# Optimization experiments

Hardware: AMD Instinct MI355X
Metric: run time of the kernel (lower is better)

Reference implementation:

```python
import jax, jax.numpy as jnp
import numpy as np

B, NUM_CLASSES, H, W, CF = 2, 19, 64, 64, 256
TOPK_IDX = 20  # hard-coded in the torch source: sorted descending value at index 20


def _cosine(x):
    # x: [B, N, D] -> clamped cosine affinity [B, N, N]
    xn = x / (jnp.linalg.norm(x, axis=2, keepdims=True) + 1e-9)
    return jnp.maximum(jnp.einsum('bnd,bmd->bnm', xn, xn), 0.0)


def _conv1x1(x, w, b):
    # x: [B, C, H, W], w: [O, C], b: [O]
    return jnp.einsum('bchw,oc->bohw', x, w) + b[None, :, None, None]


def setup_inputs() -> dict:
    key = jax.random.key(0)
    ks = jax.random.split(key, 12)
    s_c = (2.0 / NUM_CLASSES) ** 0.5  # kaiming fan_in scale for 1x1 conv
    s_f = (2.0 / CF) ** 0.5
    return {
        'pred': jax.random.normal(ks[0], (B, NUM_CLASSES, H, W), jnp.float32),
        'feat': jax.random.normal(ks[1], (B, CF, H, W), jnp.float32),
        'w_cls1': jax.random.normal(ks[2], (NUM_CLASSES, NUM_CLASSES), jnp.float32) * s_c,
        'b_cls1': jnp.zeros((NUM_CLASSES,), jnp.float32),
        'w_cls2': jax.random.normal(ks[3], (NUM_CLASSES, NUM_CLASSES), jnp.float32) * s_c,
        'b_cls2': jnp.zeros((NUM_CLASSES,), jnp.float32),
        'w_pro1': jax.random.normal(ks[4], (CF, CF), jnp.float32) * s_f,
        'b_pro1': jnp.zeros((CF,), jnp.float32),
        'w_pro2': jax.random.normal(ks[5], (CF, CF), jnp.float32) * s_f,
        'b_pro2': jnp.zeros((CF,), jnp.float32),
        'class_weight': jnp.ones((NUM_CLASSES,), jnp.float32),
    }


def reference(pred, feat, w_cls1, b_cls1, w_cls2, b_cls2,
              w_pro1, b_pro1, w_pro2, b_pro2, class_weight):
    bsz, c, h, w = feat.shape
    C = pred.shape[1]
    N = h * w
    feat_flat = feat.reshape(bsz, c, N).transpose(0, 2, 1)  # [B, N, 256]

    # --- no_grad block 1: confidence mask + top-k sparsified cosine affinity ---
    prob = jax.nn.softmax(pred, axis=1)
    p_prob = prob.max(axis=1)      # [B, H, W]
    p_max = prob.argmax(axis=1)    # [B, H, W]
    cwm = class_weight / (class_weight.max() + 1e-10) * 0.95
    mask = ((p_prob >= 0.95) | (p_prob >= cwm[p_max])).astype(jnp.float32)
    mask = jax.lax.stop_gradient(mask.reshape(bsz, N, 1))  # broadcast over classes

    aff1 = _cosine(feat_flat)                                # [B, N, N]
    thr = -jnp.sort(-aff1, axis=-1)[:, :, TOPK_IDX:TOPK_IDX + 1]  # per-row 21st largest
    aff1 = jnp.where(aff1 < thr, 0.0, aff1)
    aff1 = jax.lax.stop_gradient(aff1 + aff1.transpose(0, 2, 1))

    # --- degree-normalized propagation of predictions ---
    pred_flat = pred.reshape(bsz, C, N).transpose(0, 2, 1)   # [B, N, C]
    d1 = (aff1.sum(-1) + 1e-10) ** -0.5                      # D^{-1/2}
    aff1n = d1[:, :, None] * aff1 * d1[:, None, :]           # D^{-1/2} A D^{-1/2}
    p2 = jnp.einsum('bnm,bmc->bnc', aff1n, pred_flat)
    p3 = (0.8 * p2 + 0.2 * pred_flat) * (1.0 - mask) + (0.2 * p2 + 0.8 * pred_flat) * mask
    pred2 = p3.transpose(0, 2, 1).reshape(bsz, C, h, w)
    pred_out = _conv1x1(_conv1x1(pred2, w_cls1, b_cls1), w_cls2, b_cls2)

    # --- no_grad block 2: class-consistency-masked affinity over refined softmax ---
    oh = jax.nn.one_hot(p_max, C, dtype=jnp.float32)         # [B, H, W, C]
    # faithful to torch: permute(0,2,3,1) on the already-[B,H,W,C] one-hot, then flat view
    oh = jnp.transpose(oh, (0, 2, 3, 1)).reshape(bsz, -1, C)
    sp = jax.nn.softmax(pred_out, axis=1).reshape(bsz, C, N).transpose(0, 2, 1)
    aff_f = _cosine(sp)
    aff_f = jnp.where(_cosine(oh) == 0.0, 0.0, aff_f)
    d2 = (aff_f.sum(-1) + 1e-10) ** -0.5
    aff_fn = jax.lax.stop_gradient(d2[:, :, None] * aff_f * d2[:, None, :])

    # --- propagate features and project ---
    new_feat = jnp.einsum('bnm,bmc->bnc', aff_fn, feat_flat)
    new_feat = new_feat.transpose(0, 2, 1).reshape(bsz, c, h, w)
    feat_out = _conv1x1(jax.nn.relu(_conv1x1(new_feat, w_pro1, b_pro1)), w_pro2, b_pro2)
    return pred_out, feat_out
```

## Files before the change

kernel.cpp:

```cpp
#include <hip/hip_runtime.h>

#define NN 4096
#define DD 256
#define CC 19
#define BB 2
#define KSPLIT 4

typedef __attribute__((ext_vector_type(8))) short bf16x8;
typedef _Float16 f16x8 __attribute__((ext_vector_type(8)));
typedef __attribute__((ext_vector_type(4))) float f32x4;

#define GLL16(gp, lp) __builtin_amdgcn_global_load_lds( \
    (const __attribute__((address_space(1))) unsigned int*)(gp), \
    (__attribute__((address_space(3))) unsigned int*)(lp), 16, 0, 0)

__device__ inline unsigned short f2b(float f) {
  unsigned int u = __float_as_uint(f);
  return (unsigned short)((u + 0x7FFFu + ((u >> 16) & 1u)) >> 16);
}
__device__ inline float b2f(unsigned short h) {
  return __uint_as_float(((unsigned int)h) << 16);
}
__device__ inline unsigned int pack2(float a, float b) {
  return (unsigned int)f2b(a) | ((unsigned int)f2b(b) << 16);
}
__device__ inline void split16(float x, unsigned short& h, unsigned short& l) {
  _Float16 hh = (_Float16)x;
  float hf = (float)hh;
  _Float16 ll = (_Float16)((x - hf) * 2048.0f);
  h = *reinterpret_cast<unsigned short*>(&hh);
  l = *reinterpret_cast<unsigned short*>(&ll);
}

__global__ void k_mask_bits(const float* __restrict__ pred, const float* __restrict__ cw,
                            float* __restrict__ maskb, unsigned int* __restrict__ ohbits) {
  int g = blockIdx.x * 256 + threadIdx.x;
  if (g >= BB * NN) return;
  int b = g >> 12, n = g & (NN - 1);
  const float* p = pred + (size_t)b * CC * NN + n;
  float v[CC];
  float mx = -1e30f; int am = 0;
#pragma unroll
  for (int c = 0; c < CC; ++c) {
    float t = p[(size_t)c * NN];
    v[c] = t;
    if (t > mx) { mx = t; am = c; }
  }
  float s = 0.f;
#pragma unroll
  for (int c = 0; c < CC; ++c) s += expf(v[c] - mx);
  float pprob = 1.f / s;
  float cmax = 0.f;
#pragma unroll
  for (int c = 0; c < CC; ++c) cmax = fmaxf(cmax, cw[c]);
  float cwm = cw[am] / (cmax + 1e-10f) * 0.95f;
  maskb[g] = (pprob >= 0.95f || pprob >= cwm) ? 1.f : 0.f;
  int h = n >> 6, w = n & 63;
  int L = w * (CC * 64) + am * 64 + h;
  atomicOr(&ohbits[b * NN + L / CC], 1u << (L % CC));
}

__global__ void k_norm_feat(const float* __restrict__ feat,
                            unsigned short* __restrict__ xh, unsigned short* __restrict__ xl) {
  int g = blockIdx.x * 64 + threadIdx.x;
  int b = g >> 12, n = g & (NN - 1);
  const float* f = feat + (size_t)b * DD * NN + n;
  float s = 0.f;
  for (int d = 0; d < DD; ++d) { float t = f[(size_t)d * NN]; s += t * t; }
  float r = 1.f / (sqrtf(s) + 1e-9f);
  size_t ob = ((size_t)b * NN + n) * DD;
  for (int d = 0; d < DD; d += 4) {
    ushort4 oh, ol;
    split16(f[(size_t)d * NN] * r, oh.x, ol.x);
    split16(f[(size_t)(d + 1) * NN] * r, oh.y, ol.y);
    split16(f[(size_t)(d + 2) * NN] * r, oh.z, ol.z);
    split16(f[(size_t)(d + 3) * NN] * r, oh.w, ol.w);
    *reinterpret_cast<ushort4*>(&xh[ob + d]) = oh;
    *reinterpret_cast<ushort4*>(&xl[ob + d]) = ol;
  }
}

__global__ __launch_bounds__(256, 2) void k_gram1(const unsigned short* __restrict__ xh,
                                                  const unsigned short* __restrict__ xl,
                                                  float* __restrict__ M) {
  int L = blockIdx.x;
  int b = blockIdx.y;
  int I = 0;
  while (L >= 32 - I) { L -= 32 - I; ++I; }
  int J = I + L;
  int i0 = I * 128, j0 = J * 128;
  float* Mb = M + (size_t)b * NN * NN;
  const unsigned short* XH = xh + (size_t)b * NN * DD;
  const unsigned short* XL = xl + (size_t)b * NN * DD;
  __shared__ unsigned short stage[2][4][128][32];
  int t = threadIdx.x;
  int wave = t >> 6, lane = t & 63;
  int wr = (wave & 1) * 64, wc = (wave >> 1) * 64;
  int lrow = lane & 15, quad = lane >> 4;
  int sel = (lrow >> 1) & 3;
  f32x4 accH[4][4] = {}, accL[4][4] = {};
  const unsigned short* src = (wave == 0) ? XH + (size_t)i0 * DD
                             : (wave == 1) ? XL + (size_t)i0 * DD
                             : (wave == 2) ? XH + (size_t)j0 * DD
                                           : XL + (size_t)j0 * DD;
  int srow = lane >> 2;
  int spart = (lane & 3) ^ ((lane >> 3) & 3);
#pragma unroll
  for (int e = 0; e < 8; ++e)
    GLL16(&src[(size_t)(e * 16 + srow) * DD + spart * 8], &stage[0][wave][e * 16][0]);
  __syncthreads();
  int cur = 0;
  for (int k0 = 0; k0 < DD; k0 += 32) {
    if (k0 + 32 < DD) {
#pragma unroll
      for (int e = 0; e < 8; ++e)
        GLL16(&src[(size_t)(e * 16 + srow) * DD + k0 + 32 + spart * 8],
              &stage[cur ^ 1][wave][e * 16][0]);
    }
    f16x8 ah[4], al[4], bh[4], bl[4];
#pragma unroll
    for (int i = 0; i < 4; ++i) {
      int ra = wr + i * 16 + lrow;
      int rb = wc + i * 16 + lrow;
      int sl = (quad ^ sel) * 8;
      ah[i] = *reinterpret_cast<const f16x8*>(&stage[cur][0][ra][sl]);
      al[i] = *reinterpret_cast<const f16x8*>(&stage[cur][1][ra][sl]);
      bh[i] = *reinterpret_cast<const f16x8*>(&stage[cur][2][rb][sl]);
      bl[i] = *reinterpret_cast<const f16x8*>(&stage[cur][3][rb][sl]);
    }
#pragma unroll
    for (int i = 0; i < 4; ++i) {
#pragma unroll
      for (int j = 0; j < 4; ++j) {
        accH[i][j] = __builtin_amdgcn_mfma_f32_16x16x32_f16(ah[i], bh[j], accH[i][j], 0, 0, 0);
        accL[i][j] = __builtin_amdgcn_mfma_f32_16x16x32_f16(ah[i], bl[j], accL[i][j], 0, 0, 0);
        accL[i][j] = __builtin_amdgcn_mfma_f32_16x16x32_f16(al[i], bh[j], accL[i][j], 0, 0, 0);
      }
    }
    __syncthreads();
    cur ^= 1;
  }
#pragma unroll
  for (int i = 0; i < 4; ++i)
#pragma unroll
    for (int j = 0; j < 4; ++j)
#pragma unroll
      for (int reg = 0; reg < 4; ++reg)
        accH[i][j][reg] = fmaxf(accH[i][j][reg] + accL[i][j][reg] * 4.8828125e-4f, 0.f);
  float* buf = (float*)stage;
  int rr = t >> 4, cc = t & 15;
  for (int half = 0; half < 2; ++half) {
    __syncthreads();
    if ((wr >> 6) == half) {
#pragma unroll
      for (int i = 0; i < 4; ++i)
#pragma unroll
        for (int j = 0; j < 4; ++j)
#pragma unroll
          for (int reg = 0; reg < 4; ++reg)
            buf[(i * 16 + quad * 4 + reg) * 132 + wc + j * 16 + lrow] = accH[i][j][reg];
    }
    __syncthreads();
#pragma unroll
    for (int i = 0; i < 4; ++i) {
      int row = rr + i * 16;
#pragma unroll
      for (int q = 0; q < 2; ++q) {
        int col = cc * 4 + q * 64;
        *reinterpret_cast<float4*>(&Mb[(size_t)(i0 + half * 64 + row) * NN + j0 + col]) =
            *reinterpret_cast<float4*>(&buf[row * 132 + col]);
      }
    }
  }
  if (I != J) {
    for (int half = 0; half < 2; ++half) {
      __syncthreads();
      if ((wc >> 6) == half) {
#pragma unroll
        for (int i = 0; i < 4; ++i)
#pragma unroll
          for (int j = 0; j < 4; ++j)
#pragma unroll
            for (int reg = 0; reg < 4; ++reg)
              buf[(j * 16 + lrow) * 132 + wr + i * 16 + quad * 4 + reg] = accH[i][j][reg];
      }
      __syncthreads();
#pragma unroll
      for (int i = 0; i < 4; ++i) {
        int row = rr + i * 16;
#pragma unroll
        for (int q = 0; q < 2; ++q) {
          int col = cc * 4 + q * 64;
          *reinterpret_cast<float4*>(&Mb[(size_t)(j0 + half * 64 + row) * NN + i0 + col]) =
              *reinterpret_cast<float4*>(&buf[row * 132 + col]);
        }
      }
    }
  }
}

__global__ __launch_bounds__(256, 2) void k_topk(const float* __restrict__ M,
                                                 float* __restrict__ thr) {
  __shared__ unsigned int cbuf[4][64];
  int b = blockIdx.y;
  int wave = threadIdx.x >> 6, lane = threadIdx.x & 63;
  int n = blockIdx.x * 4 + wave;
  const float* row = M + (size_t)b * NN * NN + (size_t)n * NN;
  uint4 v[16];
#pragma unroll
  for (int e = 0; e < 16; ++e) {
    unsigned long long addr = (unsigned long long)(row + lane * 4 + e * 256);
    asm volatile("global_load_dwordx4 %0, %1, off" : "=v"(v[e]) : "v"(addr));
  }
  asm volatile("s_waitcnt vmcnt(0)" ::: "memory");
  __builtin_amdgcn_sched_barrier(0);
  unsigned int mx = 0u;
#pragma unroll
  for (int e = 0; e < 16; ++e) {
    unsigned int a = v[e].x > v[e].y ? v[e].x : v[e].y;
    unsigned int c2 = v[e].z > v[e].w ? v[e].z : v[e].w;
    a = a > c2 ? a : c2;
    mx = mx > a ? mx : a;
  }
  unsigned int lo = 0u, hi = 0x3FC00000u;
  while (lo < hi) {
    unsigned int mid = lo + ((hi - lo + 1) >> 1);
    if (__popcll(__ballot(mx >= mid)) >= 21) lo = mid; else hi = mid - 1;
  }
  unsigned int s = lo;
  unsigned int base = 0;
  unsigned long long ltmask = (1ull << lane) - 1ull;
#pragma unroll
  for (int e = 0; e < 16; ++e) {
#pragma unroll
    for (int q = 0; q < 4; ++q) {
      unsigned int val = (q == 0) ? v[e].x : (q == 1) ? v[e].y : (q == 2) ? v[e].z : v[e].w;
      unsigned long long mk = __ballot(val >= s);
      if (mk) {
        unsigned int pos = base + (unsigned int)__popcll(mk & ltmask);
        if (val >= s && pos < 64u) cbuf[wave][pos] = val;
        base += (unsigned int)__popcll(mk);
      }
    }
  }
  asm volatile("s_waitcnt lgkmcnt(0)" ::: "memory");
  __builtin_amdgcn_sched_barrier(0);
  unsigned int t = s;
  if (base <= 64u) {
    unsigned int cand = (lane < (int)base) ? cbuf[wave][lane] : 0u;
    lo = s; hi = 0x3FC00000u;
    while (lo < hi) {
      unsigned int mid = lo + ((hi - lo + 1) >> 1);
      if (__popcll(__ballot(cand >= mid)) >= 21) lo = mid; else hi = mid - 1;
    }
    t = lo;
  }
  {
    unsigned int t1 = t + 1u;
    int c1 = 0, c2 = 0;
#pragma unroll
    for (int e = 0; e < 16; ++e) {
      c1 += (int)__popcll(__ballot(v[e].x >= t));
      c1 += (int)__popcll(__ballot(v[e].y >= t));
      c1 += (int)__popcll(__ballot(v[e].z >= t));
      c1 += (int)__popcll(__ballot(v[e].w >= t));
      c2 += (int)__popcll(__ballot(v[e].x >= t1));
      c2 += (int)__popcll(__ballot(v[e].y >= t1));
      c2 += (int)__popcll(__ballot(v[e].z >= t1));
      c2 += (int)__popcll(__ballot(v[e].w >= t1));
    }
    if (!(c1 >= 21 && c2 < 21)) {
      lo = 0u; hi = 0x40000000u;
      while (lo < hi) {
        unsigned int mid = lo + ((hi - lo + 1) >> 1);
        int c = 0;
#pragma unroll
        for (int e = 0; e < 16; ++e) {
          c += (int)__popcll(__ballot(v[e].x >= mid));
          c += (int)__popcll(__ballot(v[e].y >= mid));
          c += (int)__popcll(__ballot(v[e].z >= mid));
          c += (int)__popcll(__ballot(v[e].w >= mid));
        }
        if (c >= 21) lo = mid; else hi = mid - 1;
      }
      t = lo;
    }
  }
  if (lane == 0) thr[b * NN + n] = __uint_as_float(t);
}

__global__ __launch_bounds__(256) void k_symm(float* __restrict__ M, const float* __restrict__ thr,
                                              float* __restrict__ dsum) {
  int L = blockIdx.x;
  int b = blockIdx.y;
  int I = 0;
  while (L >= 64 - I) { L -= 64 - I; ++I; }
  int J = I + L;
  float* Mb = M + (size_t)b * NN * NN;
  unsigned short* Mus = (unsigned short*)Mb;
  const float* th = thr + b * NN;
  __shared__ float A[64][65];
  int t = threadIdx.x;
  int i0 = I * 64, j0 = J * 64;
  float areg[16];
#pragma unroll
  for (int e = 0; e < 16; ++e) {
    int lin = t + e * 256;
    int i = lin >> 6, j = lin & 63;
    areg[e] = Mb[(size_t)(i0 + i) * NN + j0 + j];
  }
#pragma unroll
  for (int e = 0; e < 16; ++e) {
    int lin = t + e * 256;
    int i = lin >> 6, j = lin & 63;
    float a = areg[e];
    float v = a * ((a >= th[i0 + i] ? 1.f : 0.f) + (a >= th[j0 + j] ? 1.f : 0.f));
    A[i][j] = v;
  }
  __syncthreads();
  {
    int i = t >> 2, seg = (t & 3) * 16;
    float v[16];
#pragma unroll
    for (int q = 0; q < 4; ++q)
      *reinterpret_cast<float4*>(&v[q * 4]) = *reinterpret_cast<float4*>(&A[i][seg + q * 4]);
    unsigned int pk[8];
#pragma unroll
    for (int q = 0; q < 8; ++q) pk[q] = pack2(v[2 * q], v[2 * q + 1]);
    size_t ub = 2 * (size_t)(i0 + i) * NN + 2 * (size_t)j0 + seg;
    *reinterpret_cast<int4*>(&Mus[ub])     = *reinterpret_cast<int4*>(&pk[0]);
    *reinterpret_cast<int4*>(&Mus[ub + 8]) = *reinterpret_cast<int4*>(&pk[4]);
  }
  if (I != J) {
    int j = t >> 2, seg = (t & 3) * 16;
    float v[16];
#pragma unroll
    for (int e = 0; e < 16; ++e) v[e] = A[seg + e][j];
    unsigned int pk[8];
#pragma unroll
    for (int q = 0; q < 8; ++q) pk[q] = pack2(v[2 * q], v[2 * q + 1]);
    size_t ub = 2 * (size_t)(j0 + j) * NN + 2 * (size_t)i0 + seg;
    *reinterpret_cast<int4*>(&Mus[ub])     = *reinterpret_cast<int4*>(&pk[0]);
    *reinterpret_cast<int4*>(&Mus[ub + 8]) = *reinterpret_cast<int4*>(&pk[4]);
  }
  if (t < 64) {
    float s = 0.f;
#pragma unroll
    for (int j = 0; j < 64; ++j) s += A[t][j];
    atomicAdd(&dsum[b * NN + i0 + t], s);
  } else if (t < 128 && I != J) {
    int j = t - 64;
    float s = 0.f;
#pragma unroll
    for (int i = 0; i < 64; ++i) s += A[i][j];
    atomicAdd(&dsum[b * NN + j0 + j], s);
  }
}

__global__ void k_fin_d(float* __restrict__ d) {
  int g = blockIdx.x * 256 + threadIdx.x;
  if (g < BB * NN) d[g] = 1.f / sqrtf(d[g] + 1e-10f);
}

__global__ void k_make_yb(const float* __restrict__ pred, const float* __restrict__ d1,
                          unsigned short* __restrict__ ybh) {
  int g = blockIdx.x * 256 + threadIdx.x;
  int idx = g * 4;
  int b = idx / (32 * NN);
  int c = (idx / NN) & 31;
  int n = idx & (NN - 1);
  ushort4 o = make_ushort4(0, 0, 0, 0);
  if (c < CC) {
    float4 p = *reinterpret_cast<const float4*>(&pred[((size_t)b * CC + c) * NN + n]);
    const float* dd = d1 + b * NN + n;
    o.x = f2b(p.x * dd[0]); o.y = f2b(p.y * dd[1]);
    o.z = f2b(p.z * dd[2]); o.w = f2b(p.w * dd[3]);
  }
  *reinterpret_cast<ushort4*>(&ybh[idx]) = o;
}

__global__ __launch_bounds__(256) void k_p2_mfma(
    const float* __restrict__ M, const unsigned short* __restrict__ ybh,
    const float* __restrict__ d1, float* __restrict__ p2b) {
  int b = blockIdx.y;
  int n0 = blockIdx.x * 64;
  const unsigned short* Mus = (const unsigned short*)(M + (size_t)b * NN * NN);
  const unsigned short* Y = ybh + (size_t)b * 32 * NN;
  __shared__ unsigned short As[64][72];
  __shared__ unsigned short Ys[32][72];
  int t = threadIdx.x;
  int wave = t >> 6, lane = t & 63;
  int wn = (wave & 1) * 32;
  int wc = (wave >> 1) * 16;
  int lrow = lane & 15, quad = lane >> 4;
  f32x4 acc[2] = {{0.f,0.f,0.f,0.f},{0.f,0.f,0.f,0.f}};
  int sr = t >> 3, scc = (t & 7) * 8;
  for (int m0 = 0; m0 < NN; m0 += 64) {
#pragma unroll
    for (int e = 0; e < 2; ++e) {
      int rr = sr + e * 32;
      *reinterpret_cast<int4*>(&As[rr][scc]) =
          *reinterpret_cast<const int4*>(&Mus[2 * (size_t)(n0 + rr) * NN + 2 * (size_t)m0 + scc]);
    }
    *reinterpret_cast<int4*>(&Ys[sr][scc]) =
        *reinterpret_cast<const int4*>(&Y[(size_t)sr * NN + m0 + scc]);
    __syncthreads();
#pragma unroll
    for (int kc = 0; kc < 2; ++kc) {
      int ko = kc * 32 + quad * 8;
      bf16x8 bfr = *reinterpret_cast<const bf16x8*>(&Ys[wc + lrow][ko]);
#pragma unroll
      for (int i = 0; i < 2; ++i) {
        bf16x8 af = *reinterpret_cast<const bf16x8*>(&As[wn + i * 16 + lrow][ko]);
        acc[i] = __builtin_amdgcn_mfma_f32_16x16x32_bf16(af, bfr, acc[i], 0, 0, 0);
      }
    }
    __syncthreads();
  }
  int c = wc + lrow;
  if (c < CC) {
#pragma unroll
    for (int i = 0; i < 2; ++i) {
#pragma unroll
      for (int reg = 0; reg < 4; ++reg) {
        int n = n0 + wn + i * 16 + quad * 4 + reg;
        p2b[((size_t)b * NN + n) * CC + c] = d1[b * NN + n] * acc[i][reg];
      }
    }
  }
}

__global__ __launch_bounds__(256) void k_pred_head(const float* __restrict__ pred,
    const float* __restrict__ p2b, const float* __restrict__ maskb,
    const float* __restrict__ w1, const float* __restrict__ b1,
    const float* __restrict__ w2, const float* __restrict__ b2,
    float* __restrict__ out, float* __restrict__ spnT) {
  __shared__ float sw1[CC * CC], sw2[CC * CC], sb1[CC], sb2[CC];
  int t = threadIdx.x;
  for (int i = t; i < CC * CC; i += 256) { sw1[i] = w1[i]; sw2[i] = w2[i]; }
  if (t < CC) { sb1[t] = b1[t]; sb2[t] = b2[t]; }
  __syncthreads();
  int g = blockIdx.x * 256 + t;
  int b = g >> 12, n = g & (NN - 1);
  float m = maskb[g];
  float ca = (m > 0.5f) ? 0.2f : 0.8f;
  float cb = (m > 0.5f) ? 0.8f : 0.2f;
  const float* P = pred + (size_t)b * CC * NN + n;
  const float* Q = p2b + (size_t)g * CC;
  float p3[CC];
#pragma unroll
  for (int c = 0; c < CC; ++c) p3[c] = ca * Q[c] + cb * P[(size_t)c * NN];
  float midv[CC];
#pragma unroll
  for (int o = 0; o < CC; ++o) {
    float s = sb1[o];
#pragma unroll
    for (int c = 0; c < CC; ++c) s += sw1[o * CC + c] * p3[c];
    midv[o] = s;
  }
  float ov[CC];
  float mx = -1e30f;
#pragma unroll
  for (int o = 0; o < CC; ++o) {
    float s = sb2[o];
#pragma unroll
    for (int c = 0; c < CC; ++c) s += sw2[o * CC + c] * midv[c];
    ov[o] = s;
    out[(size_t)b * CC * NN + (size_t)o * NN + n] = s;
    mx = fmaxf(mx, s);
  }
  float se = 0.f;
  float e[CC];
#pragma unroll
  for (int o = 0; o < CC; ++o) { e[o] = expf(ov[o] - mx); se += e[o]; }
  float inv = 1.f / se;
  float nrm = 0.f;
#pragma unroll
  for (int o = 0; o < CC; ++o) { float sp = e[o] * inv; e[o] = sp; nrm += sp * sp; }
  float rn = 1.f / (sqrtf(nrm) + 1e-9f);
#pragma unroll
  for (int o = 0; o < CC; ++o) spnT[(size_t)b * CC * NN + (size_t)o * NN + n] = e[o] * rn;
}

__global__ __launch_bounds__(256) void k_gram2(const float* __restrict__ spnT,
    const unsigned int* __restrict__ bits, unsigned short* __restrict__ Mh) {
  int L = blockIdx.x;
  int b = blockIdx.y;
  int I = 0;
  while (L >= 64 - I) { L -= 64 - I; ++I; }
  int J = I + L;
  const float* X = spnT + (size_t)b * CC * NN;
  unsigned short* Mb = Mh + (size_t)b * NN * NN;
  __shared__ float sA[CC][64], sB[CC][64];
  __shared__ unsigned int bI[64], bJ[64];
  __shared__ float tr[64][65];
  int t = threadIdx.x;
  int r = t >> 4, c = t & 15;
  int i0 = I * 64, j0 = J * 64;
  for (int e = t; e < CC * 64; e += 256) {
    int k = e >> 6, col = e & 63;
    sA[k][col] = X[(size_t)k * NN + i0 + col];
    sB[k][col] = X[(size_t)k * NN + j0 + col];
  }
  if (t < 64) bI[t] = bits[b * NN + i0 + t];
  else if (t < 128) bJ[t - 64] = bits[b * NN + j0 + t - 64];
  __syncthreads();
  float acc[4][4] = {};
#pragma unroll
  for (int k = 0; k < CC; ++k) {
    float av[4], bv[4];
#pragma unroll
    for (int i = 0; i < 4; ++i) av[i] = sA[k][r * 4 + i];
#pragma unroll
    for (int j = 0; j < 4; ++j) bv[j] = sB[k][c * 4 + j];
#pragma unroll
    for (int i = 0; i < 4; ++i) {
#pragma unroll
      for (int j = 0; j < 4; ++j) acc[i][j] += av[i] * bv[j];
    }
  }
#pragma unroll
  for (int i = 0; i < 4; ++i) {
#pragma unroll
    for (int j = 0; j < 4; ++j) {
      bool keep = (bI[r * 4 + i] & bJ[c * 4 + j]) != 0u;
      acc[i][j] = keep ? fmaxf(acc[i][j], 0.f) : 0.f;
    }
    ushort4 v;
    v.x = f2b(acc[i][0]); v.y = f2b(acc[i][1]); v.z = f2b(acc[i][2]); v.w = f2b(acc[i][3]);
    *reinterpret_cast<ushort4*>(&Mb[(size_t)(i0 + r * 4 + i) * NN + j0 + c * 4]) = v;
  }
  if (I != J) {
#pragma unroll
    for (int i = 0; i < 4; ++i) {
#pragma unroll
      for (int j = 0; j < 4; ++j) tr[r * 4 + i][c * 4 + j] = acc[i][j];
    }
    __syncthreads();
#pragma unroll
    for (int e = 0; e < 16; ++e) {
      int lin = t + e * 256;
      int jr = lin >> 6, ic = lin & 63;
      Mb[(size_t)(j0 + jr) * NN + i0 + ic] = f2b(tr[ic][jr]);
    }
  }
}

__global__ __launch_bounds__(256) void k_rowsum2h(const unsigned short* __restrict__ Mh,
                                                  float* __restrict__ d2) {
  int b = blockIdx.y, n = blockIdx.x;
  const unsigned short* row = Mh + (size_t)b * NN * NN + (size_t)n * NN;
  int t = threadIdx.x;
  float s = 0.f;
#pragma unroll
  for (int i = 0; i < 8; ++i) {
    unsigned int u = *reinterpret_cast<const unsigned int*>(&row[(i * 256 + t) * 2]);
    s += __uint_as_float(u << 16) + __uint_as_float(u & 0xffff0000u);
  }
  for (int off = 32; off > 0; off >>= 1) s += __shfl_down(s, off);
  __shared__ float p4[4];
  int wid = t >> 6, lane = t & 63;
  if (lane == 0) p4[wid] = s;
  __syncthreads();
  if (t == 0) d2[b * NN + n] = 1.f / sqrtf(p4[0] + p4[1] + p4[2] + p4[3] + 1e-10f);
}

__global__ void k_make_z(const float* __restrict__ feat, const float* __restrict__ d2,
                         unsigned short* __restrict__ zb) {
  int g = blockIdx.x * 256 + threadIdx.x;
  int idx = g * 4;
  int b = idx / (DD * NN);
  int m = idx & (NN - 1);
  float4 f = *reinterpret_cast<const float4*>(&feat[idx]);
  const float* dd = d2 + b * NN + m;
  ushort4 o;
  o.x = f2b(f.x * dd[0]); o.y = f2b(f.y * dd[1]);
  o.z = f2b(f.z * dd[2]); o.w = f2b(f.w * dd[3]);
  *reinterpret_cast<ushort4*>(&zb[idx]) = o;
}

__global__ void k_prep_w(const float* __restrict__ w1, const float* __restrict__ w2,
                         unsigned short* __restrict__ wb1, unsigned short* __restrict__ wb2) {
  int g = blockIdx.x * 256 + threadIdx.x;
  wb1[g] = f2b(w1[g]);
  wb2[g] = f2b(w2[g]);
}

__global__ __launch_bounds__(256) void k_newfeat_mfma(
    const unsigned short* __restrict__ Mh, const unsigned short* __restrict__ zb,
    float* __restrict__ nfp) {
  int zz = blockIdx.z;
  int b = zz / KSPLIT, ks = zz % KSPLIT;
  int nblk = blockIdx.x;
  int dblk = blockIdx.y;
  const int KLEN = NN / KSPLIT;
  const unsigned short* A = zb + (size_t)b * DD * NN + (size_t)(dblk * 64) * NN + ks * KLEN;
  const unsigned short* Bm = Mh + (size_t)b * NN * NN + (size_t)(nblk * 64) * NN + ks * KLEN;
  __shared__ unsigned short As[64][72];
  __shared__ unsigned short Bs[64][72];
  int t = threadIdx.x;
  int wave = t >> 6, lane = t & 63;
  int wd = (wave & 1) * 32, wn = (wave >> 1) * 32;
  int lrow = lane & 15, quad = lane >> 4;
  f32x4 acc[2][2] = {{{0.f,0.f,0.f,0.f},{0.f,0.f,0.f,0.f}},{{0.f,0.f,0.f,0.f},{0.f,0.f,0.f,0.f}}};
  int sr = t >> 3, sc = (t & 7) * 8;
  for (int m0 = 0; m0 < KLEN; m0 += 64) {
#pragma unroll
    for (int e = 0; e < 2; ++e) {
      int rr = sr + e * 32;
      *reinterpret_cast<int4*>(&As[rr][sc]) =
          *reinterpret_cast<const int4*>(&A[(size_t)rr * NN + m0 + sc]);
      *reinterpret_cast<int4*>(&Bs[rr][sc]) =
          *reinterpret_cast<const int4*>(&Bm[(size_t)rr * NN + m0 + sc]);
    }
    __syncthreads();
#pragma unroll
    for (int kc = 0; kc < 2; ++kc) {
      int ko = kc * 32 + quad * 8;
      bf16x8 af[2], bfr[2];
#pragma unroll
      for (int i = 0; i < 2; ++i) {
        af[i]  = *reinterpret_cast<const bf16x8*>(&As[wd + i * 16 + lrow][ko]);
        bfr[i] = *reinterpret_cast<const bf16x8*>(&Bs[wn + i * 16 + lrow][ko]);
      }
#pragma unroll
      for (int i = 0; i < 2; ++i)
#pragma unroll
        for (int j = 0; j < 2; ++j)
          acc[i][j] = __builtin_amdgcn_mfma_f32_16x16x32_bf16(af[i], bfr[j], acc[i][j], 0, 0, 0);
    }
    __syncthreads();
  }
#pragma unroll
  for (int j = 0; j < 2; ++j) {
    int n = nblk * 64 + wn + j * 16 + lrow;
#pragma unroll
    for (int i = 0; i < 2; ++i) {
      int d = dblk * 64 + wd + i * 16 + quad * 4;
      float4 v = make_float4(acc[i][j].x, acc[i][j].y, acc[i][j].z, acc[i][j].w);
      *reinterpret_cast<float4*>(&nfp[((size_t)zz * NN + n) * DD + d]) = v;
    }
  }
}

__global__ void k_nf_reduce(const float* __restrict__ nfp, const float* __restrict__ d2,
                            unsigned short* __restrict__ nfh) {
  int g = blockIdx.x * 256 + threadIdx.x;
  int idx = g * 4;
  int b = idx / (NN * DD);
  int n = (idx / DD) & (NN - 1);
  size_t base = (size_t)idx + (size_t)b * (KSPLIT - 1) * NN * DD;
  float4 s = make_float4(0.f, 0.f, 0.f, 0.f);
#pragma unroll
  for (int ks = 0; ks < KSPLIT; ++ks) {
    float4 v = *reinterpret_cast<const float4*>(&nfp[base + (size_t)ks * NN * DD]);
    s.x += v.x; s.y += v.y; s.z += v.z; s.w += v.w;
  }
  float sc = d2[b * NN + n];
  ushort4 o;
  o.x = f2b(s.x * sc); o.y = f2b(s.y * sc); o.z = f2b(s.z * sc); o.w = f2b(s.w * sc);
  *reinterpret_cast<ushort4*>(&nfh[idx]) = o;
}

__global__ __launch_bounds__(256) void k_conv1_mfma(
    const unsigned short* __restrict__ nfh, const unsigned short* __restrict__ wb1,
    const float* __restrict__ b1, unsigned short* __restrict__ midh) {
  int b = blockIdx.z;
  int nblk = blockIdx.x;
  int oblk = blockIdx.y;
  int n0 = nblk * 64, o0 = oblk * 64;
  __shared__ unsigned short As[64][72];
  __shared__ unsigned short Bs[64][72];
  int t = threadIdx.x;
  int wave = t >> 6, lane = t & 63;
  int wn = (wave & 1) * 32, wo = (wave >> 1) * 32;
  int lrow = lane & 15, quad = lane >> 4;
  f32x4 acc[2][2] = {{{0.f,0.f,0.f,0.f},{0.f,0.f,0.f,0.f}},{{0.f,0.f,0.f,0.f},{0.f,0.f,0.f,0.f}}};
  int sr = t >> 3, sc = (t & 7) * 8;
  for (int d0 = 0; d0 < DD; d0 += 64) {
#pragma unroll
    for (int e = 0; e < 2; ++e) {
      int rr = sr + e * 32;
      *reinterpret_cast<int4*>(&As[rr][sc]) =
          *reinterpret_cast<const int4*>(&nfh[((size_t)b * NN + n0 + rr) * DD + d0 + sc]);
      *reinterpret_cast<int4*>(&Bs[rr][sc]) =
          *reinterpret_cast<const int4*>(&wb1[(size_t)(o0 + rr) * DD + d0 + sc]);
    }
    __syncthreads();
#pragma unroll
    for (int kc = 0; kc < 2; ++kc) {
      int ko = kc * 32 + quad * 8;
      bf16x8 af[2], bfr[2];
#pragma unroll
      for (int i = 0; i < 2; ++i) {
        af[i]  = *reinterpret_cast<const bf16x8*>(&As[wn + i * 16 + lrow][ko]);
        bfr[i] = *reinterpret_cast<const bf16x8*>(&Bs[wo + i * 16 + lrow][ko]);
      }
#pragma unroll
      for (int i = 0; i < 2; ++i)
#pragma unroll
        for (int j = 0; j < 2; ++j)
          acc[i][j] = __builtin_amdgcn_mfma_f32_16x16x32_bf16(af[i], bfr[j], acc[i][j], 0, 0, 0);
    }
    __syncthreads();
  }
#pragma unroll
  for (int j = 0; j < 2; ++j) {
    int o = o0 + wo + j * 16 + lrow;
    float bias = b1[o];
#pragma unroll
    for (int i = 0; i < 2; ++i) {
      int nb = n0 + wn + i * 16 + quad * 4;
      ushort4 v;
      v.x = f2b(fmaxf(acc[i][j].x + bias, 0.f));
      v.y = f2b(fmaxf(acc[i][j].y + bias, 0.f));
      v.z = f2b(fmaxf(acc[i][j].z + bias, 0.f));
      v.w = f2b(fmaxf(acc[i][j].w + bias, 0.f));
      *reinterpret_cast<ushort4*>(&midh[((size_t)b * DD + o) * NN + nb]) = v;
    }
  }
}

__global__ __launch_bounds__(256) void k_conv2_mfma(
    const unsigned short* __restrict__ midh, const unsigned short* __restrict__ wb2,
    const float* __restrict__ b2, float* __restrict__ outp) {
  int b = blockIdx.z;
  int nblk = blockIdx.x;
  int oblk = blockIdx.y;
  int n0 = nblk * 64, o0 = oblk * 64;
  __shared__ unsigned short As[64][72];
  __shared__ unsigned short Bs[64][72];
  int t = threadIdx.x;
  int wave = t >> 6, lane = t & 63;
  int wn = (wave & 1) * 32, wo = (wave >> 1) * 32;
  int lrow = lane & 15, quad = lane >> 4;
  f32x4 acc[2][2] = {{{0.f,0.f,0.f,0.f},{0.f,0.f,0.f,0.f}},{{0.f,0.f,0.f,0.f},{0.f,0.f,0.f,0.f}}};
  int sr = t >> 3, sc = (t & 7) * 8;
  for (int d0 = 0; d0 < DD; d0 += 64) {
#pragma unroll
    for (int e = 0; e < 2; ++e) {
      int rr = sr + e * 32;
      *reinterpret_cast<int4*>(&Bs[rr][sc]) =
          *reinterpret_cast<const int4*>(&wb2[(size_t)(o0 + rr) * DD + d0 + sc]);
      unsigned short v[8];
      *reinterpret_cast<int4*>(v) =
          *reinterpret_cast<const int4*>(&midh[((size_t)b * DD + d0 + rr) * NN + n0 + sc]);
#pragma unroll
      for (int j = 0; j < 8; ++j) As[sc + j][rr] = v[j];
    }
    __syncthreads();
#pragma unroll
    for (int kc = 0; kc < 2; ++kc) {
      int ko = kc * 32 + quad * 8;
      bf16x8 af[2], bfr[2];
#pragma unroll
      for (int i = 0; i < 2; ++i) {
        af[i]  = *reinterpret_cast<const bf16x8*>(&As[wn + i * 16 + lrow][ko]);
        bfr[i] = *reinterpret_cast<const bf16x8*>(&Bs[wo + i * 16 + lrow][ko]);
      }
#pragma unroll
      for (int i = 0; i < 2; ++i)
#pragma unroll
        for (int j = 0; j < 2; ++j)
          acc[i][j] = __builtin_amdgcn_mfma_f32_16x16x32_bf16(af[i], bfr[j], acc[i][j], 0, 0, 0);
    }
    __syncthreads();
  }
#pragma unroll
  for (int j = 0; j < 2; ++j) {
    int o = o0 + wo + j * 16 + lrow;
    float bias = b2[o];
#pragma unroll
    for (int i = 0; i < 2; ++i) {
      int nb = n0 + wn + i * 16 + quad * 4;
      float4 v = make_float4(acc[i][j].x + bias, acc[i][j].y + bias,
                             acc[i][j].z + bias, acc[i][j].w + bias);
      *reinterpret_cast<float4*>(&outp[((size_t)b * DD + o) * NN + nb]) = v;
    }
  }
}

extern "C" void kernel_launch(void* const* d_in, const int* in_sizes, int n_in,
                              void* d_out, int out_size, void* d_ws, size_t ws_size,
                              hipStream_t stream) {
  (void)in_sizes; (void)n_in; (void)out_size; (void)ws_size;
  const float* pred   = (const float*)d_in[0];
  const float* feat   = (const float*)d_in[1];
  const float* w_cls1 = (const float*)d_in[2];
  const float* b_cls1 = (const float*)d_in[3];
  const float* w_cls2 = (const float*)d_in[4];
  const float* b_cls2 = (const float*)d_in[5];
  const float* w_pro1 = (const float*)d_in[6];
  const float* b_pro1 = (const float*)d_in[7];
  const float* w_pro2 = (const float*)d_in[8];
  const float* b_pro2 = (const float*)d_in[9];
  const float* cw     = (const float*)d_in[10];
  float* out = (float*)d_out;

  float* Mbuf = (float*)d_ws;
  float* spnT = Mbuf + (size_t)BB * NN * NN;
  float* p2b  = spnT + (size_t)BB * CC * NN;
  float* thr  = p2b + (size_t)BB * NN * CC;
  float* dsum = thr + BB * NN;
  float* d2s  = dsum + BB * NN;
  float* maskb = d2s + BB * NN;
  unsigned int* ohbits = (unsigned int*)(maskb + BB * NN);
  unsigned short* xh   = (unsigned short*)(ohbits + BB * NN);
  unsigned short* xl   = xh + (size_t)BB * NN * DD;
  unsigned short* nfh  = xl + (size_t)BB * NN * DD;
  unsigned short* midh = nfh + (size_t)BB * NN * DD;
  unsigned short* zb   = midh + (size_t)BB * DD * NN;
  unsigned short* wb1  = zb + (size_t)BB * DD * NN;
  unsigned short* wb2  = wb1 + (size_t)DD * DD;
  unsigned short* ybh  = wb2 + (size_t)DD * DD;
  unsigned short* Mh   = (unsigned short*)Mbuf;
  float* nfp = (float*)(Mh + (size_t)BB * NN * NN);

  hipMemsetAsync(dsum, 0, sizeof(float) * BB * NN, stream);
  hipMemsetAsync(ohbits, 0, sizeof(unsigned int) * BB * NN, stream);

  k_mask_bits<<<BB * NN / 256, 256, 0, stream>>>(pred, cw, maskb, ohbits);
  k_norm_feat<<<BB * NN / 64, 64, 0, stream>>>(feat, xh, xl);
  k_gram1<<<dim3(528, BB), 256, 0, stream>>>(xh, xl, Mbuf);
  k_topk<<<dim3(NN / 4, BB), 256, 0, stream>>>(Mbuf, thr);
  k_symm<<<dim3(2080, BB), 256, 0, stream>>>(Mbuf, thr, dsum);
  k_fin_d<<<BB * NN / 256, 256, 0, stream>>>(dsum);
  k_make_yb<<<BB * 32 * NN / 4 / 256, 256, 0, stream>>>(pred, dsum, ybh);
  k_p2_mfma<<<dim3(NN / 64, BB), 256, 0, stream>>>(Mbuf, ybh, dsum, p2b);
  k_pred_head<<<BB * NN / 256, 256, 0, stream>>>(pred, p2b, maskb, w_cls1, b_cls1,
                                                 w_cls2, b_cls2, out, spnT);
  k_gram2<<<dim3(2080, BB), 256, 0, stream>>>(spnT, ohbits, Mh);
  k_rowsum2h<<<dim3(NN, BB), 256, 0, stream>>>(Mh, d2s);
  k_make_z<<<BB * DD * NN / 4 / 256, 256, 0, stream>>>(feat, d2s, zb);
  k_prep_w<<<DD * DD / 256, 256, 0, stream>>>(w_pro1, w_pro2, wb1, wb2);
  k_newfeat_mfma<<<dim3(64, 4, BB * KSPLIT), 256, 0, stream>>>(Mh, zb, nfp);
  k_nf_reduce<<<BB * NN * DD / 4 / 256, 256, 0, stream>>>(nfp, d2s, nfh);
  k_conv1_mfma<<<dim3(64, 4, BB), 256, 0, stream>>>(nfh, wb1, b_pro1, midh);
  k_conv2_mfma<<<dim3(64, 4, BB), 256, 0, stream>>>(midh, wb2, b_pro2,
                                                    out + (size_t)BB * CC * NN);
}
```

Measured before the change: 385.5 us.

## Double-buffer newfeat GEMM tiles via direct global-to-LDS loads with XOR swizzle

The newfeat MFMA kernel now loads its A and B tiles straight into LDS with global_load_lds, double-buffered so the next K-slice is prefetched while the current one is multiplied. Padding is replaced by an XOR swizzle on the 16-byte chunk index to avoid bank conflicts, and launch bounds request two blocks per CU. The goal is to hide global memory latency and cut register round-trips. It relies on the async LDS writes being complete at the single barrier per iteration, which is a correctness risk without an explicit vmcnt wait.

```diff
diff --git a/kernel.cpp b/kernel.cpp
--- a/kernel.cpp
+++ b/kernel.cpp
@@ -586,7 +586,7 @@
   wb2[g] = f2b(w2[g]);
 }
 
-__global__ __launch_bounds__(256) void k_newfeat_mfma(
+__global__ __launch_bounds__(256, 2) void k_newfeat_mfma(
     const unsigned short* __restrict__ Mh, const unsigned short* __restrict__ zb,
     float* __restrict__ nfp) {
   int zz = blockIdx.z;
@@ -596,32 +596,41 @@
   const int KLEN = NN / KSPLIT;
   const unsigned short* A = zb + (size_t)b * DD * NN + (size_t)(dblk * 64) * NN + ks * KLEN;
   const unsigned short* Bm = Mh + (size_t)b * NN * NN + (size_t)(nblk * 64) * NN + ks * KLEN;
-  __shared__ unsigned short As[64][72];
-  __shared__ unsigned short Bs[64][72];
+  __shared__ unsigned short As[2][64][64];
+  __shared__ unsigned short Bs[2][64][64];
   int t = threadIdx.x;
   int wave = t >> 6, lane = t & 63;
   int wd = (wave & 1) * 32, wn = (wave >> 1) * 32;
   int lrow = lane & 15, quad = lane >> 4;
   f32x4 acc[2][2] = {{{0.f,0.f,0.f,0.f},{0.f,0.f,0.f,0.f}},{{0.f,0.f,0.f,0.f},{0.f,0.f,0.f,0.f}}};
-  int sr = t >> 3, sc = (t & 7) * 8;
+  int lr3 = lane >> 3;
+  int srow = wave * 8 + lr3;
+  int spart = (lane & 7) ^ lr3;
+#pragma unroll
+  for (int e = 0; e < 2; ++e) {
+    GLL16(&A [(size_t)(e * 32 + srow) * NN + spart * 8], &As[0][e * 32 + wave * 8][0]);
+    GLL16(&Bm[(size_t)(e * 32 + srow) * NN + spart * 8], &Bs[0][e * 32 + wave * 8][0]);
+  }
+  __syncthreads();
+  int cur = 0;
   for (int m0 = 0; m0 < KLEN; m0 += 64) {
-#pragma unroll
-    for (int e = 0; e < 2; ++e) {
-      int rr = sr + e * 32;
-      *reinterpret_cast<int4*>(&As[rr][sc]) =
-          *reinterpret_cast<const int4*>(&A[(size_t)rr * NN + m0 + sc]);
-      *reinterpret_cast<int4*>(&Bs[rr][sc]) =
-          *reinterpret_cast<const int4*>(&Bm[(size_t)rr * NN + m0 + sc]);
-    }
-    __syncthreads();
+    if (m0 + 64 < KLEN) {
+#pragma unroll
+      for (int e = 0; e < 2; ++e) {
+        GLL16(&A [(size_t)(e * 32 + srow) * NN + m0 + 64 + spart * 8],
+              &As[cur ^ 1][e * 32 + wave * 8][0]);
+        GLL16(&Bm[(size_t)(e * 32 + srow) * NN + m0 + 64 + spart * 8],
+              &Bs[cur ^ 1][e * 32 + wave * 8][0]);
+      }
+    }
 #pragma unroll
     for (int kc = 0; kc < 2; ++kc) {
-      int ko = kc * 32 + quad * 8;
+      int sl = ((kc * 4 + quad) ^ (lrow & 7)) * 8;
       bf16x8 af[2], bfr[2];
 #pragma unroll
       for (int i = 0; i < 2; ++i) {
-        af[i]  = *reinterpret_cast<const bf16x8*>(&As[wd + i * 16 + lrow][ko]);
-        bfr[i] = *reinterpret_cast<const bf16x8*>(&Bs[wn + i * 16 + lrow][ko]);
+        af[i]  = *reinterpret_cast<const bf16x8*>(&As[cur][wd + i * 16 + lrow][sl]);
+        bfr[i] = *reinterpret_cast<const bf16x8*>(&Bs[cur][wn + i * 16 + lrow][sl]);
       }
 #pragma unroll
       for (int i = 0; i < 2; ++i)
@@ -630,6 +639,7 @@
           acc[i][j] = __builtin_amdgcn_mfma_f32_16x16x32_bf16(af[i], bfr[j], acc[i][j], 0, 0, 0);
     }
     __syncthreads();
+    cur ^= 1;
   }
 #pragma unroll
   for (int j = 0; j < 2; ++j) {
```

Result: faster. 362.9 us (-5.9%).
